# Kernel optimization log

Measured on AMD Instinct MI355X. Metric: run time of the kernel, lower is better.

Reference implementation:

```python
import jax, jax.numpy as jnp
import numpy as np

N, E, F_IN, C, H = 50000, 800000, 256, 128, 2
NEG_SLOPE = 0.2


def setup_inputs() -> dict:
    key = jax.random.key(0)
    ks = jax.random.split(key, 8)
    x = jax.random.normal(ks[0], (N, F_IN), dtype=jnp.float32)
    edge_index = jax.random.randint(ks[1], (2, E), 0, N, dtype=jnp.int64)
    # GATConv params (PyG: lin weight [H*C, F_IN], att_src/att_dst [H, C], bias [H*C])
    s_lin = 1.0 / np.sqrt(F_IN)
    W = jax.random.uniform(ks[2], (H * C, F_IN), minval=-s_lin, maxval=s_lin, dtype=jnp.float32)
    att_src = jax.random.normal(ks[3], (H, C), dtype=jnp.float32) * 0.1
    att_dst = jax.random.normal(ks[4], (H, C), dtype=jnp.float32) * 0.1
    bias = jnp.zeros((H * C,), dtype=jnp.float32)
    # trailing nn.Linear(H*C, C)
    s_l = 1.0 / np.sqrt(H * C)
    lin_w = jax.random.uniform(ks[5], (C, H * C), minval=-s_l, maxval=s_l, dtype=jnp.float32)
    lin_b = jax.random.uniform(ks[6], (C,), minval=-s_l, maxval=s_l, dtype=jnp.float32)
    return {"x": x, "edge_index": edge_index, "W": W, "att_src": att_src,
            "att_dst": att_dst, "bias": bias, "lin_w": lin_w, "lin_b": lin_b}


def _gat_forward(x, edge_index, W, att_src, att_dst, bias, lin_w, lin_b):
    # add self-loops (PyG default add_self_loops=True)
    loop = jnp.arange(N, dtype=edge_index.dtype)
    src = jnp.concatenate([edge_index[0], loop])  # [E+N]
    dst = jnp.concatenate([edge_index[1], loop])  # [E+N]

    h = (x @ W.T).reshape(N, H, C)                # [N, H, C]
    a_src = jnp.einsum('nhc,hc->nh', h, att_src)  # [N, H]
    a_dst = jnp.einsum('nhc,hc->nh', h, att_dst)  # [N, H]

    e = a_src[src] + a_dst[dst]                   # [E+N, H]
    e = jnp.where(e > 0, e, NEG_SLOPE * e)        # LeakyReLU(0.2)

    # softmax over edges grouped by destination node
    m = jax.ops.segment_max(e, dst, num_segments=N)          # [N, H]
    m = jnp.where(jnp.isfinite(m), m, 0.0)
    ex = jnp.exp(e - jax.lax.stop_gradient(m)[dst])
    denom = jax.ops.segment_sum(ex, dst, num_segments=N)     # [N, H]
    alpha = ex / jnp.maximum(denom[dst], 1e-16)               # [E+N, H]

    msg = h[src] * alpha[:, :, None]                          # [E+N, H, C]
    out = jax.ops.segment_sum(msg, dst, num_segments=N)       # [N, H, C]
    out = out.reshape(N, H * C) + bias

    out = jax.nn.elu(out)
    return out @ lin_w.T + lin_b                               # [N, C]


def reference(x, edge_index, W, att_src, att_dst, bias, lin_w, lin_b):
    return _gat_forward(x, edge_index, W, att_src, att_dst, bias, lin_w, lin_b)
```

## Files before the change

### kernel.cpp

```cpp
#include <hip/hip_runtime.h>
#include <math.h>

#define NN 50000
#define EE 800000
#define ET (EE + NN)
#define FIN 256
#define CCOUT 128
#define HH 2
#define HC 256
#define NEG 0.2f

#define NB_EDGE ((ET + 255) / 256)
#define NB_SCAN ((NN + 255) / 256)

typedef __attribute__((ext_vector_type(8))) short short8;
typedef __attribute__((ext_vector_type(4))) float floatx4;

__device__ __forceinline__ unsigned short f2bf(float f)
{
    union { float f; unsigned int u; } x; x.f = f;
    unsigned int r = x.u + 0x7fffu + ((x.u >> 16) & 1u);
    return (unsigned short)(r >> 16);
}
__device__ __forceinline__ float bf2f(unsigned short u)
{
    union { unsigned int u; float f; } x; x.u = ((unsigned int)u) << 16;
    return x.f;
}

__global__ void detect_kernel(const int* __restrict__ ei32, int* __restrict__ flag)
{
    if (threadIdx.x == 0 && blockIdx.x == 0) {
        int is64 = 1;
        for (int k = 0; k < 32; k++) {
            if (ei32[2 * k + 1] != 0) { is64 = 0; break; }
        }
        *flag = is64;
    }
}

__device__ __forceinline__ int load_idx(const int* ei32, int is64, int pos)
{
    return is64 ? ei32[2 * pos] : ei32[pos];
}

__global__ __launch_bounds__(256) void watt_kernel(const float* __restrict__ W,
                                                   const float* __restrict__ att_s,
                                                   const float* __restrict__ att_d,
                                                   float* __restrict__ ws,
                                                   float* __restrict__ wd)
{
    int hd = blockIdx.x;
    int f = threadIdx.x;
    float as = 0.f, ad = 0.f;
    for (int c = 0; c < CCOUT; c++) {
        float wv = W[(size_t)(hd * CCOUT + c) * FIN + f];
        as += att_s[hd * CCOUT + c] * wv;
        ad += att_d[hd * CCOUT + c] * wv;
    }
    ws[hd * FIN + f] = as;
    wd[hd * FIN + f] = ad;
}

__global__ __launch_bounds__(256) void xprep_kernel(const float* __restrict__ x,
                                                    const float* __restrict__ was,
                                                    const float* __restrict__ wad,
                                                    unsigned short* __restrict__ xb,
                                                    float* __restrict__ a_s,
                                                    float* __restrict__ a_d)
{
    int t = threadIdx.x;
    int w = t >> 6, l = t & 63;
    int n = blockIdx.x * 4 + w;
    float4 xv = *(const float4*)(x + (size_t)n * FIN + l * 4);
    ushort4 xs;
    xs.x = f2bf(xv.x); xs.y = f2bf(xv.y); xs.z = f2bf(xv.z); xs.w = f2bf(xv.w);
    *(ushort4*)(xb + (size_t)n * FIN + l * 4) = xs;

    float4 s0 = *(const float4*)(was + l * 4);
    float4 s1 = *(const float4*)(was + FIN + l * 4);
    float4 d0 = *(const float4*)(wad + l * 4);
    float4 d1 = *(const float4*)(wad + FIN + l * 4);
    float vs0 = xv.x * s0.x + xv.y * s0.y + xv.z * s0.z + xv.w * s0.w;
    float vs1 = xv.x * s1.x + xv.y * s1.y + xv.z * s1.z + xv.w * s1.w;
    float vd0 = xv.x * d0.x + xv.y * d0.y + xv.z * d0.z + xv.w * d0.w;
    float vd1 = xv.x * d1.x + xv.y * d1.y + xv.z * d1.z + xv.w * d1.w;
#pragma unroll
    for (int off = 32; off > 0; off >>= 1) {
        vs0 += __shfl_down(vs0, off);
        vs1 += __shfl_down(vs1, off);
        vd0 += __shfl_down(vd0, off);
        vd1 += __shfl_down(vd1, off);
    }
    if (l == 0) {
        a_s[n * 2 + 0] = vs0; a_s[n * 2 + 1] = vs1;
        a_d[n * 2 + 0] = vd0; a_d[n * 2 + 1] = vd1;
    }
}

__global__ __launch_bounds__(256) void convw_kernel(const float* __restrict__ src,
                                                    unsigned short* __restrict__ dst, int n4)
{
    int i = blockIdx.x * 256 + threadIdx.x;
    if (i >= n4) return;
    float4 v = *(const float4*)(src + (size_t)i * 4);
    ushort4 o;
    o.x = f2bf(v.x); o.y = f2bf(v.y); o.z = f2bf(v.z); o.w = f2bf(v.w);
    *(ushort4*)(dst + (size_t)i * 4) = o;
}

template <bool ADD_BIAS, bool OUT_BF16>
__global__ __launch_bounds__(256) void gemm_mfma(const unsigned short* __restrict__ A,
                                                 const unsigned short* __restrict__ B,
                                                 const float* __restrict__ bias,
                                                 void* __restrict__ Cout,
                                                 int M, int N, int K)
{
    const int LDT = 40;
    __shared__ unsigned short As[128 * LDT];
    __shared__ unsigned short Bs[128 * LDT];

    int tid = threadIdx.x;
    int wave = tid >> 6, lane = tid & 63;
    int wr = wave >> 1, wc = wave & 1;
    int quad = lane >> 4, l16 = lane & 15;
    int bm0 = blockIdx.x * 128;
    int bn0 = blockIdx.y * 128;

    floatx4 acc[4][4] = {};

    for (int kk = 0; kk < K; kk += 32) {
#pragma unroll
        for (int p = 0; p < 2; p++) {
            int idx = p * 256 + tid;
            int row = idx >> 2, seg = idx & 3;
            int grow = bm0 + row; if (grow >= M) grow = M - 1;
            uint4 va = *(const uint4*)(A + (size_t)grow * K + kk + seg * 8);
            *(uint4*)(&As[row * LDT + seg * 8]) = va;
            uint4 vb = *(const uint4*)(B + (size_t)(bn0 + row) * K + kk + seg * 8);
            *(uint4*)(&Bs[row * LDT + seg * 8]) = vb;
        }
        __syncthreads();

        short8 af[4], bfr[4];
#pragma unroll
        for (int mi = 0; mi < 4; mi++)
            af[mi] = *(const short8*)(&As[(wr * 64 + mi * 16 + l16) * LDT + quad * 8]);
#pragma unroll
        for (int ni = 0; ni < 4; ni++)
            bfr[ni] = *(const short8*)(&Bs[(wc * 64 + ni * 16 + l16) * LDT + quad * 8]);
#pragma unroll
        for (int mi = 0; mi < 4; mi++)
#pragma unroll
            for (int ni = 0; ni < 4; ni++)
                acc[mi][ni] = __builtin_amdgcn_mfma_f32_16x16x32_bf16(af[mi], bfr[ni], acc[mi][ni], 0, 0, 0);
        __syncthreads();
    }

#pragma unroll
    for (int mi = 0; mi < 4; mi++) {
#pragma unroll
        for (int ni = 0; ni < 4; ni++) {
            int col = bn0 + wc * 64 + ni * 16 + l16;
#pragma unroll
            for (int r = 0; r < 4; r++) {
                int row = bm0 + wr * 64 + mi * 16 + quad * 4 + r;
                if (row < M) {
                    float v = acc[mi][ni][r];
                    if (ADD_BIAS) v += bias[col];
                    if (OUT_BF16)
                        ((unsigned short*)Cout)[(size_t)row * N + col] = f2bf(v);
                    else
                        ((float*)Cout)[(size_t)row * N + col] = v;
                }
            }
        }
    }
}

__global__ void count_kernel(const int* __restrict__ ei32, const int* __restrict__ flag,
                             int* __restrict__ deg, int* __restrict__ eord)
{
    int e = blockIdx.x * blockDim.x + threadIdx.x;
    if (e >= ET) return;
    int is64 = *flag;
    int d = (e < EE) ? load_idx(ei32, is64, EE + e) : (e - EE);
    eord[e] = atomicAdd(&deg[d], 1);
}

__global__ __launch_bounds__(256) void scan1(const int* __restrict__ deg,
                                             int* __restrict__ tmp, int* __restrict__ bsum)
{
    __shared__ int s[256];
    int i = blockIdx.x * 256 + threadIdx.x;
    int v = (i < NN) ? deg[i] : 0;
    s[threadIdx.x] = v;
    __syncthreads();
    for (int off = 1; off < 256; off <<= 1) {
        int add = (threadIdx.x >= off) ? s[threadIdx.x - off] : 0;
        __syncthreads();
        s[threadIdx.x] += add;
        __syncthreads();
    }
    if (i < NN) tmp[i] = s[threadIdx.x];
    if (threadIdx.x == 255) bsum[blockIdx.x] = s[255];
}

__global__ __launch_bounds__(256) void scan2(int* __restrict__ bsum)
{
    __shared__ int s[256];
    int t = threadIdx.x;
    int v = (t < NB_SCAN) ? bsum[t] : 0;
    s[t] = v;
    __syncthreads();
    for (int off = 1; off < 256; off <<= 1) {
        int add = (t >= off) ? s[t - off] : 0;
        __syncthreads();
        s[t] += add;
        __syncthreads();
    }
    if (t < NB_SCAN) bsum[t] = s[t] - v;
}

__global__ __launch_bounds__(256) void scan3(const int* __restrict__ deg,
                                             const int* __restrict__ tmp,
                                             const int* __restrict__ bsum,
                                             int* __restrict__ rowstart)
{
    int i = blockIdx.x * 256 + threadIdx.x;
    if (i < NN) rowstart[i] = tmp[i] - deg[i] + bsum[blockIdx.x];
    if (i == 0) rowstart[NN] = ET;
}

__global__ void scatter_kernel(const int* __restrict__ ei32, const int* __restrict__ flag,
                               const int* __restrict__ eord,
                               const int* __restrict__ rowstart,
                               int* __restrict__ csr_src)
{
    int e = blockIdx.x * blockDim.x + threadIdx.x;
    if (e >= ET) return;
    int is64 = *flag;
    int s, d;
    if (e < EE) { s = load_idx(ei32, is64, e); d = load_idx(ei32, is64, EE + e); }
    else { s = d = e - EE; }
    csr_src[rowstart[d] + eord[e]] = s;
}

__global__ __launch_bounds__(256) void agg3_kernel(const unsigned short* __restrict__ hb,
                                                   const int* __restrict__ rowstart,
                                                   const int* __restrict__ csr_src,
                                                   const float* __restrict__ a_s,
                                                   const float* __restrict__ a_d,
                                                   const float* __restrict__ bias,
                                                   unsigned short* __restrict__ aggb)
{
    int wave = threadIdx.x >> 6, lane = threadIdx.x & 63;
    int d = blockIdx.x * 4 + wave;
    int head = lane >> 5;
    int c = (lane & 31) * 4 + head * 128;
    float a_dv = a_d[d * 2 + head];
    int j0 = rowstart[d], j1 = rowstart[d + 1];

    float acc0 = 0.f, acc1 = 0.f, acc2 = 0.f, acc3 = 0.f, psum = 0.f;

    int j = j0;
    for (; j + 3 < j1; j += 4) {
        int s0 = csr_src[j], s1 = csr_src[j + 1], s2 = csr_src[j + 2], s3 = csr_src[j + 3];
        float e0 = a_s[s0 * 2 + head] + a_dv;
        float e1 = a_s[s1 * 2 + head] + a_dv;
        float e2 = a_s[s2 * 2 + head] + a_dv;
        float e3 = a_s[s3 * 2 + head] + a_dv;
        e0 = e0 > 0.f ? e0 : NEG * e0;
        e1 = e1 > 0.f ? e1 : NEG * e1;
        e2 = e2 > 0.f ? e2 : NEG * e2;
        e3 = e3 > 0.f ? e3 : NEG * e3;
        float p0 = __expf(e0), p1 = __expf(e1), p2 = __expf(e2), p3 = __expf(e3);
        psum += p0 + p1 + p2 + p3;
        uint2 h0 = *(const uint2*)(hb + (size_t)s0 * HC + c);
        uint2 h1 = *(const uint2*)(hb + (size_t)s1 * HC + c);
        uint2 h2 = *(const uint2*)(hb + (size_t)s2 * HC + c);
        uint2 h3 = *(const uint2*)(hb + (size_t)s3 * HC + c);
        acc0 += p0 * bf2f((unsigned short)h0.x) + p1 * bf2f((unsigned short)h1.x)
              + p2 * bf2f((unsigned short)h2.x) + p3 * bf2f((unsigned short)h3.x);
        acc1 += p0 * bf2f((unsigned short)(h0.x >> 16)) + p1 * bf2f((unsigned short)(h1.x >> 16))
              + p2 * bf2f((unsigned short)(h2.x >> 16)) + p3 * bf2f((unsigned short)(h3.x >> 16));
        acc2 += p0 * bf2f((unsigned short)h0.y) + p1 * bf2f((unsigned short)h1.y)
              + p2 * bf2f((unsigned short)h2.y) + p3 * bf2f((unsigned short)h3.y);
        acc3 += p0 * bf2f((unsigned short)(h0.y >> 16)) + p1 * bf2f((unsigned short)(h1.y >> 16))
              + p2 * bf2f((unsigned short)(h2.y >> 16)) + p3 * bf2f((unsigned short)(h3.y >> 16));
    }
    for (; j < j1; j++) {
        int s0 = csr_src[j];
        float e0 = a_s[s0 * 2 + head] + a_dv;
        e0 = e0 > 0.f ? e0 : NEG * e0;
        float p0 = __expf(e0);
        psum += p0;
        uint2 h0 = *(const uint2*)(hb + (size_t)s0 * HC + c);
        acc0 += p0 * bf2f((unsigned short)h0.x);
        acc1 += p0 * bf2f((unsigned short)(h0.x >> 16));
        acc2 += p0 * bf2f((unsigned short)h0.y);
        acc3 += p0 * bf2f((unsigned short)(h0.y >> 16));
    }

    float inv = 1.f / fmaxf(psum, 1e-16f);
    float v0 = acc0 * inv + bias[c + 0];
    float v1 = acc1 * inv + bias[c + 1];
    float v2 = acc2 * inv + bias[c + 2];
    float v3 = acc3 * inv + bias[c + 3];
    v0 = v0 > 0.f ? v0 : expm1f(v0);
    v1 = v1 > 0.f ? v1 : expm1f(v1);
    v2 = v2 > 0.f ? v2 : expm1f(v2);
    v3 = v3 > 0.f ? v3 : expm1f(v3);
    ushort4 o;
    o.x = f2bf(v0); o.y = f2bf(v1); o.z = f2bf(v2); o.w = f2bf(v3);
    *(ushort4*)(aggb + (size_t)d * HC + c) = o;
}

extern "C" void kernel_launch(void* const* d_in, const int* in_sizes, int n_in,
                              void* d_out, int out_size, void* d_ws, size_t ws_size,
                              hipStream_t stream)
{
    const float* x       = (const float*)d_in[0];
    const int*   ei32    = (const int*)d_in[1];
    const float* W       = (const float*)d_in[2];
    const float* att_src = (const float*)d_in[3];
    const float* att_dst = (const float*)d_in[4];
    const float* bias    = (const float*)d_in[5];
    const float* lin_w   = (const float*)d_in[6];
    const float* lin_b   = (const float*)d_in[7];
    float* out = (float*)d_out;

    char* ws = (char*)d_ws;
    size_t off = 0;
    auto alloc = [&](size_t bytes) -> void* {
        void* p = ws + off;
        off += (bytes + 255) & ~(size_t)255;
        return p;
    };

    int*   deg    = (int*)alloc((size_t)NN * 4);
    size_t zero_bytes = off;

    int*   flag     = (int*)alloc(256);
    int*   tmp      = (int*)alloc((size_t)NN * 4);
    int*   bsum     = (int*)alloc(1024);
    int*   rowstart = (int*)alloc((size_t)(NN + 1) * 4);
    int*   eord     = (int*)alloc((size_t)ET * 4);
    float* was      = (float*)alloc((size_t)HH * FIN * 4);
    float* wad      = (float*)alloc((size_t)HH * FIN * 4);
    float* a_s      = (float*)alloc((size_t)NN * 2 * 4);
    float* a_d      = (float*)alloc((size_t)NN * 2 * 4);
    int*   csr_src  = (int*)alloc((size_t)ET * 4);
    unsigned short* xb     = (unsigned short*)alloc((size_t)NN * FIN * 2);
    unsigned short* Wb     = (unsigned short*)alloc((size_t)HC * FIN * 2);
    unsigned short* linwb  = (unsigned short*)alloc((size_t)CCOUT * HC * 2);
    unsigned short* hb     = (unsigned short*)alloc((size_t)NN * HC * 2);
    unsigned short* aggb   = (unsigned short*)alloc((size_t)NN * HC * 2);

    hipMemsetAsync(d_ws, 0, zero_bytes, stream);

    detect_kernel<<<1, 64, 0, stream>>>(ei32, flag);

    count_kernel<<<NB_EDGE, 256, 0, stream>>>(ei32, flag, deg, eord);

    watt_kernel<<<HH, 256, 0, stream>>>(W, att_src, att_dst, was, wad);

    xprep_kernel<<<NN / 4, 256, 0, stream>>>(x, was, wad, xb, a_s, a_d);

    convw_kernel<<<(HC * FIN / 4 + 255) / 256, 256, 0, stream>>>(W, Wb, HC * FIN / 4);
    convw_kernel<<<(CCOUT * HC / 4 + 255) / 256, 256, 0, stream>>>(lin_w, linwb, CCOUT * HC / 4);

    scan1<<<NB_SCAN, 256, 0, stream>>>(deg, tmp, bsum);
    scan2<<<1, 256, 0, stream>>>(bsum);
    scan3<<<NB_SCAN, 256, 0, stream>>>(deg, tmp, bsum, rowstart);

    scatter_kernel<<<NB_EDGE, 256, 0, stream>>>(ei32, flag, eord, rowstart, csr_src);

    dim3 g1((NN + 127) / 128, HC / 128);
    gemm_mfma<false, true><<<g1, 256, 0, stream>>>(xb, Wb, nullptr, hb, NN, HC, FIN);

    agg3_kernel<<<NN / 4, 256, 0, stream>>>(hb, rowstart, csr_src, a_s, a_d, bias, aggb);

    dim3 g2((NN + 127) / 128, CCOUT / 128);
    gemm_mfma<true, false><<<g2, 256, 0, stream>>>(aggb, linwb, lin_b, out, NN, CCOUT, HC);
}
```

Baseline: 284.8 us.

## Merge prep kernels and precompute edge attention weights in CSR scatter

Four small setup kernels (format detect, attention-weight fold, two weight conversions) become one multi-role prep kernel, and the x-prep and degree-count kernels are merged into a single launch. The CSR scatter now computes the LeakyReLU+exp edge scores for both heads and stores them as half2 next to the source index in an 8-byte record. The aggregation kernel then reads that record instead of gathering a_s per edge and recomputing exp. This cuts launch count and random a_s gathers, at the cost of doubling the CSR array size and storing unnormalized exp values in fp16, which may overflow or lose precision for large scores since no max is subtracted.

New measurement: 292.0 us. +2.5%, slower.

```diff
diff --git a/kernel.cpp b/kernel.cpp
--- a/kernel.cpp
+++ b/kernel.cpp
@@ -1,4 +1,5 @@
 #include <hip/hip_runtime.h>
+#include <hip/hip_fp16.h>
 #include <math.h>
 
 #define NN 50000
@@ -12,6 +13,11 @@
 
 #define NB_EDGE ((ET + 255) / 256)
 #define NB_SCAN ((NN + 255) / 256)
+#define NB_XPREP (NN / 4)
+
+#define PREP_W_BLOCKS 64
+#define PREP_LW_BLOCKS 32
+#define PREP_GRID (3 + PREP_W_BLOCKS + PREP_LW_BLOCKS)
 
 typedef __attribute__((ext_vector_type(8))) short short8;
 typedef __attribute__((ext_vector_type(4))) float floatx4;
@@ -28,85 +34,101 @@
     return x.f;
 }
 
-__global__ void detect_kernel(const int* __restrict__ ei32, int* __restrict__ flag)
-{
-    if (threadIdx.x == 0 && blockIdx.x == 0) {
-        int is64 = 1;
-        for (int k = 0; k < 32; k++) {
-            if (ei32[2 * k + 1] != 0) { is64 = 0; break; }
-        }
-        *flag = is64;
-    }
-}
-
 __device__ __forceinline__ int load_idx(const int* ei32, int is64, int pos)
 {
     return is64 ? ei32[2 * pos] : ei32[pos];
 }
 
-__global__ __launch_bounds__(256) void watt_kernel(const float* __restrict__ W,
+__global__ __launch_bounds__(256) void prep_kernel(const float* __restrict__ W,
                                                    const float* __restrict__ att_s,
                                                    const float* __restrict__ att_d,
-                                                   float* __restrict__ ws,
-                                                   float* __restrict__ wd)
-{
-    int hd = blockIdx.x;
-    int f = threadIdx.x;
-    float as = 0.f, ad = 0.f;
-    for (int c = 0; c < CCOUT; c++) {
-        float wv = W[(size_t)(hd * CCOUT + c) * FIN + f];
-        as += att_s[hd * CCOUT + c] * wv;
-        ad += att_d[hd * CCOUT + c] * wv;
-    }
-    ws[hd * FIN + f] = as;
-    wd[hd * FIN + f] = ad;
-}
-
-__global__ __launch_bounds__(256) void xprep_kernel(const float* __restrict__ x,
-                                                    const float* __restrict__ was,
-                                                    const float* __restrict__ wad,
-                                                    unsigned short* __restrict__ xb,
-                                                    float* __restrict__ a_s,
-                                                    float* __restrict__ a_d)
-{
-    int t = threadIdx.x;
-    int w = t >> 6, l = t & 63;
-    int n = blockIdx.x * 4 + w;
-    float4 xv = *(const float4*)(x + (size_t)n * FIN + l * 4);
-    ushort4 xs;
-    xs.x = f2bf(xv.x); xs.y = f2bf(xv.y); xs.z = f2bf(xv.z); xs.w = f2bf(xv.w);
-    *(ushort4*)(xb + (size_t)n * FIN + l * 4) = xs;
-
-    float4 s0 = *(const float4*)(was + l * 4);
-    float4 s1 = *(const float4*)(was + FIN + l * 4);
-    float4 d0 = *(const float4*)(wad + l * 4);
-    float4 d1 = *(const float4*)(wad + FIN + l * 4);
-    float vs0 = xv.x * s0.x + xv.y * s0.y + xv.z * s0.z + xv.w * s0.w;
-    float vs1 = xv.x * s1.x + xv.y * s1.y + xv.z * s1.z + xv.w * s1.w;
-    float vd0 = xv.x * d0.x + xv.y * d0.y + xv.z * d0.z + xv.w * d0.w;
-    float vd1 = xv.x * d1.x + xv.y * d1.y + xv.z * d1.z + xv.w * d1.w;
-#pragma unroll
-    for (int off = 32; off > 0; off >>= 1) {
-        vs0 += __shfl_down(vs0, off);
-        vs1 += __shfl_down(vs1, off);
-        vd0 += __shfl_down(vd0, off);
-        vd1 += __shfl_down(vd1, off);
-    }
-    if (l == 0) {
-        a_s[n * 2 + 0] = vs0; a_s[n * 2 + 1] = vs1;
-        a_d[n * 2 + 0] = vd0; a_d[n * 2 + 1] = vd1;
-    }
-}
-
-__global__ __launch_bounds__(256) void convw_kernel(const float* __restrict__ src,
-                                                    unsigned short* __restrict__ dst, int n4)
-{
-    int i = blockIdx.x * 256 + threadIdx.x;
-    if (i >= n4) return;
-    float4 v = *(const float4*)(src + (size_t)i * 4);
-    ushort4 o;
-    o.x = f2bf(v.x); o.y = f2bf(v.y); o.z = f2bf(v.z); o.w = f2bf(v.w);
-    *(ushort4*)(dst + (size_t)i * 4) = o;
+                                                   const float* __restrict__ lin_w,
+                                                   const int* __restrict__ ei32,
+                                                   float* __restrict__ was,
+                                                   float* __restrict__ wad,
+                                                   unsigned short* __restrict__ Wb,
+                                                   unsigned short* __restrict__ linwb,
+                                                   int* __restrict__ flag)
+{
+    int b = blockIdx.x, t = threadIdx.x;
+    if (b == 0) {
+        if (t < 64) {
+            int v = ei32[2 * t + 1];
+            unsigned long long m = __ballot(v != 0);
+            if (t == 0) *flag = (m == 0ull) ? 1 : 0;
+        }
+    } else if (b <= 2) {
+        int hd = b - 1;
+        float as = 0.f, ad = 0.f;
+        for (int c = 0; c < CCOUT; c++) {
+            float wv = W[(size_t)(hd * CCOUT + c) * FIN + t];
+            as += att_s[hd * CCOUT + c] * wv;
+            ad += att_d[hd * CCOUT + c] * wv;
+        }
+        was[hd * FIN + t] = as;
+        wad[hd * FIN + t] = ad;
+    } else if (b < 3 + PREP_W_BLOCKS) {
+        int i = (b - 3) * 256 + t;
+        float4 v = *(const float4*)(W + (size_t)i * 4);
+        ushort4 o;
+        o.x = f2bf(v.x); o.y = f2bf(v.y); o.z = f2bf(v.z); o.w = f2bf(v.w);
+        *(ushort4*)(Wb + (size_t)i * 4) = o;
+    } else {
+        int i = (b - 3 - PREP_W_BLOCKS) * 256 + t;
+        float4 v = *(const float4*)(lin_w + (size_t)i * 4);
+        ushort4 o;
+        o.x = f2bf(v.x); o.y = f2bf(v.y); o.z = f2bf(v.z); o.w = f2bf(v.w);
+        *(ushort4*)(linwb + (size_t)i * 4) = o;
+    }
+}
+
+__global__ __launch_bounds__(256) void xprep_count_kernel(const float* __restrict__ x,
+                                                          const float* __restrict__ was,
+                                                          const float* __restrict__ wad,
+                                                          unsigned short* __restrict__ xb,
+                                                          float* __restrict__ a_s,
+                                                          float* __restrict__ a_d,
+                                                          const int* __restrict__ ei32,
+                                                          const int* __restrict__ flag,
+                                                          int* __restrict__ deg,
+                                                          int* __restrict__ eord)
+{
+    int b = blockIdx.x, t = threadIdx.x;
+    if (b < NB_XPREP) {
+        int w = t >> 6, l = t & 63;
+        int n = b * 4 + w;
+        float4 xv = *(const float4*)(x + (size_t)n * FIN + l * 4);
+        ushort4 xs;
+        xs.x = f2bf(xv.x); xs.y = f2bf(xv.y); xs.z = f2bf(xv.z); xs.w = f2bf(xv.w);
+        *(ushort4*)(xb + (size_t)n * FIN + l * 4) = xs;
+
+        float4 s0 = *(const float4*)(was + l * 4);
+        float4 s1 = *(const float4*)(was + FIN + l * 4);
+        float4 d0 = *(const float4*)(wad + l * 4);
+        float4 d1 = *(const float4*)(wad + FIN + l * 4);
+        float vs0 = xv.x * s0.x + xv.y * s0.y + xv.z * s0.z + xv.w * s0.w;
+        float vs1 = xv.x * s1.x + xv.y * s1.y + xv.z * s1.z + xv.w * s1.w;
+        float vd0 = xv.x * d0.x + xv.y * d0.y + xv.z * d0.z + xv.w * d0.w;
+        float vd1 = xv.x * d1.x + xv.y * d1.y + xv.z * d1.z + xv.w * d1.w;
+#pragma unroll
+        for (int off = 32; off > 0; off >>= 1) {
+            vs0 += __shfl_down(vs0, off);
+            vs1 += __shfl_down(vs1, off);
+            vd0 += __shfl_down(vd0, off);
+            vd1 += __shfl_down(vd1, off);
+        }
+        if (l == 0) {
+            a_s[n * 2 + 0] = vs0; a_s[n * 2 + 1] = vs1;
+            a_d[n * 2 + 0] = vd0; a_d[n * 2 + 1] = vd1;
+        }
+    } else {
+        int e = (b - NB_XPREP) * 256 + t;
+        if (e < ET) {
+            int is64 = *flag;
+            int d = (e < EE) ? load_idx(ei32, is64, EE + e) : (e - EE);
+            eord[e] = atomicAdd(&deg[d], 1);
+        }
+    }
 }
 
 template <bool ADD_BIAS, bool OUT_BF16>
@@ -178,16 +200,6 @@
     }
 }
 
-__global__ void count_kernel(const int* __restrict__ ei32, const int* __restrict__ flag,
-                             int* __restrict__ deg, int* __restrict__ eord)
-{
-    int e = blockIdx.x * blockDim.x + threadIdx.x;
-    if (e >= ET) return;
-    int is64 = *flag;
-    int d = (e < EE) ? load_idx(ei32, is64, EE + e) : (e - EE);
-    eord[e] = atomicAdd(&deg[d], 1);
-}
-
 __global__ __launch_bounds__(256) void scan1(const int* __restrict__ deg,
                                              int* __restrict__ tmp, int* __restrict__ bsum)
 {
@@ -235,7 +247,9 @@
 __global__ void scatter_kernel(const int* __restrict__ ei32, const int* __restrict__ flag,
                                const int* __restrict__ eord,
                                const int* __restrict__ rowstart,
-                               int* __restrict__ csr_src)
+                               const float* __restrict__ a_s,
+                               const float* __restrict__ a_d,
+                               uint2* __restrict__ rec)
 {
     int e = blockIdx.x * blockDim.x + threadIdx.x;
     if (e >= ET) return;
@@ -243,14 +257,20 @@
     int s, d;
     if (e < EE) { s = load_idx(ei32, is64, e); d = load_idx(ei32, is64, EE + e); }
     else { s = d = e - EE; }
-    csr_src[rowstart[d] + eord[e]] = s;
-}
-
-__global__ __launch_bounds__(256) void agg3_kernel(const unsigned short* __restrict__ hb,
+    float e0 = a_s[s * 2 + 0] + a_d[d * 2 + 0];
+    float e1 = a_s[s * 2 + 1] + a_d[d * 2 + 1];
+    e0 = e0 > 0.f ? e0 : NEG * e0;
+    e1 = e1 > 0.f ? e1 : NEG * e1;
+    __half2 hp = __floats2half2_rn(__expf(e0), __expf(e1));
+    uint2 r;
+    r.x = (unsigned int)s;
+    r.y = *(unsigned int*)&hp;
+    rec[rowstart[d] + eord[e]] = r;
+}
+
+__global__ __launch_bounds__(256) void agg4_kernel(const unsigned short* __restrict__ hb,
                                                    const int* __restrict__ rowstart,
-                                                   const int* __restrict__ csr_src,
-                                                   const float* __restrict__ a_s,
-                                                   const float* __restrict__ a_d,
+                                                   const uint2* __restrict__ rec,
                                                    const float* __restrict__ bias,
                                                    unsigned short* __restrict__ aggb)
 {
@@ -258,28 +278,22 @@
     int d = blockIdx.x * 4 + wave;
     int head = lane >> 5;
     int c = (lane & 31) * 4 + head * 128;
-    float a_dv = a_d[d * 2 + head];
     int j0 = rowstart[d], j1 = rowstart[d + 1];
 
     float acc0 = 0.f, acc1 = 0.f, acc2 = 0.f, acc3 = 0.f, psum = 0.f;
 
     int j = j0;
     for (; j + 3 < j1; j += 4) {
-        int s0 = csr_src[j], s1 = csr_src[j + 1], s2 = csr_src[j + 2], s3 = csr_src[j + 3];
-        float e0 = a_s[s0 * 2 + head] + a_dv;
-        float e1 = a_s[s1 * 2 + head] + a_dv;
-        float e2 = a_s[s2 * 2 + head] + a_dv;
-        float e3 = a_s[s3 * 2 + head] + a_dv;
-        e0 = e0 > 0.f ? e0 : NEG * e0;
-        e1 = e1 > 0.f ? e1 : NEG * e1;
-        e2 = e2 > 0.f ? e2 : NEG * e2;
-        e3 = e3 > 0.f ? e3 : NEG * e3;
-        float p0 = __expf(e0), p1 = __expf(e1), p2 = __expf(e2), p3 = __expf(e3);
+        uint2 r0 = rec[j], r1 = rec[j + 1], r2 = rec[j + 2], r3 = rec[j + 3];
+        float p0 = __half2float(((const __half*)&r0.y)[head]);
+        float p1 = __half2float(((const __half*)&r1.y)[head]);
+        float p2 = __half2float(((const __half*)&r2.y)[head]);
+        float p3 = __half2float(((const __half*)&r3.y)[head]);
         psum += p0 + p1 + p2 + p3;
-        uint2 h0 = *(const uint2*)(hb + (size_t)s0 * HC + c);
-        uint2 h1 = *(const uint2*)(hb + (size_t)s1 * HC + c);
-        uint2 h2 = *(const uint2*)(hb + (size_t)s2 * HC + c);
-        uint2 h3 = *(const uint2*)(hb + (size_t)s3 * HC + c);
+        uint2 h0 = *(const uint2*)(hb + (size_t)r0.x * HC + c);
+        uint2 h1 = *(const uint2*)(hb + (size_t)r1.x * HC + c);
+        uint2 h2 = *(const uint2*)(hb + (size_t)r2.x * HC + c);
+        uint2 h3 = *(const uint2*)(hb + (size_t)r3.x * HC + c);
         acc0 += p0 * bf2f((unsigned short)h0.x) + p1 * bf2f((unsigned short)h1.x)
               + p2 * bf2f((unsigned short)h2.x) + p3 * bf2f((unsigned short)h3.x);
         acc1 += p0 * bf2f((unsigned short)(h0.x >> 16)) + p1 * bf2f((unsigned short)(h1.x >> 16))
@@ -290,12 +304,10 @@
               + p2 * bf2f((unsigned short)(h2.y >> 16)) + p3 * bf2f((unsigned short)(h3.y >> 16));
     }
     for (; j < j1; j++) {
-        int s0 = csr_src[j];
-        float e0 = a_s[s0 * 2 + head] + a_dv;
-        e0 = e0 > 0.f ? e0 : NEG * e0;
-        float p0 = __expf(e0);
+        uint2 r0 = rec[j];
+        float p0 = __half2float(((const __half*)&r0.y)[head]);
         psum += p0;
-        uint2 h0 = *(const uint2*)(hb + (size_t)s0 * HC + c);
+        uint2 h0 = *(const uint2*)(hb + (size_t)r0.x * HC + c);
         acc0 += p0 * bf2f((unsigned short)h0.x);
         acc1 += p0 * bf2f((unsigned short)(h0.x >> 16));
         acc2 += p0 * bf2f((unsigned short)h0.y);
@@ -350,7 +362,7 @@
     float* wad      = (float*)alloc((size_t)HH * FIN * 4);
     float* a_s      = (float*)alloc((size_t)NN * 2 * 4);
     float* a_d      = (float*)alloc((size_t)NN * 2 * 4);
-    int*   csr_src  = (int*)alloc((size_t)ET * 4);
+    uint2* rec      = (uint2*)alloc((size_t)ET * 8);
     unsigned short* xb     = (unsigned short*)alloc((size_t)NN * FIN * 2);
     unsigned short* Wb     = (unsigned short*)alloc((size_t)HC * FIN * 2);
     unsigned short* linwb  = (unsigned short*)alloc((size_t)CCOUT * HC * 2);
@@ -359,27 +371,22 @@
 
     hipMemsetAsync(d_ws, 0, zero_bytes, stream);
 
-    detect_kernel<<<1, 64, 0, stream>>>(ei32, flag);
-
-    count_kernel<<<NB_EDGE, 256, 0, stream>>>(ei32, flag, deg, eord);
-
-    watt_kernel<<<HH, 256, 0, stream>>>(W, att_src, att_dst, was, wad);
-
-    xprep_kernel<<<NN / 4, 256, 0, stream>>>(x, was, wad, xb, a_s, a_d);
-
-    convw_kernel<<<(HC * FIN / 4 + 255) / 256, 256, 0, stream>>>(W, Wb, HC * FIN / 4);
-    convw_kernel<<<(CCOUT * HC / 4 + 255) / 256, 256, 0, stream>>>(lin_w, linwb, CCOUT * HC / 4);
+    prep_kernel<<<PREP_GRID, 256, 0, stream>>>(W, att_src, att_dst, lin_w, ei32,
+                                               was, wad, Wb, linwb, flag);
+
+    xprep_count_kernel<<<NB_XPREP + NB_EDGE, 256, 0, stream>>>(x, was, wad, xb, a_s, a_d,
+                                                               ei32, flag, deg, eord);
 
     scan1<<<NB_SCAN, 256, 0, stream>>>(deg, tmp, bsum);
     scan2<<<1, 256, 0, stream>>>(bsum);
     scan3<<<NB_SCAN, 256, 0, stream>>>(deg, tmp, bsum, rowstart);
 
-    scatter_kernel<<<NB_EDGE, 256, 0, stream>>>(ei32, flag, eord, rowstart, csr_src);
+    scatter_kernel<<<NB_EDGE, 256, 0, stream>>>(ei32, flag, eord, rowstart, a_s, a_d, rec);
 
     dim3 g1((NN + 127) / 128, HC / 128);
     gemm_mfma<false, true><<<g1, 256, 0, stream>>>(xb, Wb, nullptr, hb, NN, HC, FIN);
 
-    agg3_kernel<<<NN / 4, 256, 0, stream>>>(hb, rowstart, csr_src, a_s, a_d, bias, aggb);
+    agg4_kernel<<<NN / 4, 256, 0, stream>>>(hb, rowstart, rec, bias, aggb);
 
     dim3 g2((NN + 127) / 128, CCOUT / 128);
     gemm_mfma<true, false><<<g2, 256, 0, stream>>>(aggb, linwb, lin_b, out, NN, CCOUT, HC);
```
